# Optimization experiments

Measured on AMD Instinct MI355X. Metric: run time of the kernel, lower is better.

The kernel has to match this reference:

```python
import jax, jax.numpy as jnp
import numpy as np

NUM_GRAPHS = 512

def gcn_conv(x, src, dst, W, b, n):
    # x: [N, Fin], W: [Fin, Fout]. PyG GCNConv: add self loops, symmetric norm.
    h = x @ W  # [N, Fout]
    loop = jnp.arange(n)
    s = jnp.concatenate([src, loop])
    d = jnp.concatenate([dst, loop])
    ones = jnp.ones(s.shape[0], dtype=h.dtype)
    deg = jax.ops.segment_sum(ones, d, num_segments=n)  # includes self loop -> >= 1
    dinv = jax.lax.rsqrt(deg)
    norm = dinv[s] * dinv[d]  # [E+N]
    msg = h[s] * norm[:, None]  # gather + scale (memory-bound)
    out = jax.ops.segment_sum(msg, d, num_segments=n)
    return out + b

def setup_inputs() -> dict:
    key = jax.random.key(0)
    ks = jax.random.split(key, 10)
    N, E, F, H, O, EF = 100000, 1600000, 128, 128, 1, 16
    x = jax.random.normal(ks[0], (N, F), dtype=jnp.float32)
    edge_index = jax.random.randint(ks[1], (2, E), 0, N)
    edge_attr = jax.random.normal(ks[2], (E, EF), dtype=jnp.float32)
    batch = jnp.sort(jax.random.randint(ks[3], (N,), 0, NUM_GRAPHS))
    s1 = 1.0 / np.sqrt(F)
    s2 = 1.0 / np.sqrt(H)
    W1 = jax.random.uniform(ks[4], (F, H), jnp.float32, -s1, s1)
    b1 = jnp.zeros((H,), jnp.float32)
    W2 = jax.random.uniform(ks[5], (H, H), jnp.float32, -s2, s2)
    b2 = jnp.zeros((H,), jnp.float32)
    Wl = jax.random.uniform(ks[6], (H, O), jnp.float32, -s2, s2)
    bl = jnp.zeros((O,), jnp.float32)
    return {"x": x, "edge_index": edge_index, "edge_attr": edge_attr, "batch": batch,
            "W1": W1, "b1": b1, "W2": W2, "b2": b2, "Wl": Wl, "bl": bl}

def reference(x, edge_index, edge_attr, batch, W1, b1, W2, b2, Wl, bl):
    n = x.shape[0]
    src, dst = edge_index[0], edge_index[1]
    h = jax.nn.relu(gcn_conv(x, src, dst, W1, b1, n))
    h = gcn_conv(h, src, dst, W2, b2, n)
    # global mean pool by graph id
    summed = jax.ops.segment_sum(h, batch, num_segments=NUM_GRAPHS)  # [G, H]
    counts = jax.ops.segment_sum(jnp.ones((n,), h.dtype), batch, num_segments=NUM_GRAPHS)
    pooled = summed / jnp.maximum(counts, 1.0)[:, None]
    return pooled @ Wl + bl  # [G, 1]
```

## Files before the change

kernel.cpp:

```cpp
#include <hip/hip_runtime.h>


typedef __attribute__((ext_vector_type(8))) short short8;
typedef __attribute__((ext_vector_type(4))) float f32x4;

#define CHUNK 4096
#define RW    128
#define SCAP  6144
#define JCAP  512
#define WCAP  6144

__device__ __forceinline__ unsigned short bf16r(float f) {
    unsigned u = __float_as_uint(f);
    u += 0x7FFFu + ((u >> 16) & 1u);
    return (unsigned short)(u >> 16);
}

__device__ __forceinline__ float bff(unsigned short u) {
    return __uint_as_float((unsigned)u << 16);
}

__global__ __launch_bounds__(256) void k_partw(
    const int* __restrict__ src, const int* __restrict__ dst,
    int* __restrict__ part, int* __restrict__ off_t, int* __restrict__ cnt_t,
    const float* __restrict__ W1, unsigned short* __restrict__ w1p,
    const float* __restrict__ W2, const float* __restrict__ Wl,
    float* __restrict__ w2l, int E, int nchunks, int NR)
{
    int tid = threadIdx.x;
    if (blockIdx.x >= nchunks) {
        int b = blockIdx.x - nchunks;
        if (b == 64) {
            if (tid < 128) {
                float s = 0.0f;
                for (int j = 0; j < 128; ++j) s = fmaf(W2[tid * 128 + j], Wl[j], s);
                w2l[tid] = s;
            }
            return;
        }
        int idx = b * 256 + tid;
        int k = idx >> 7, n = idx & 127;
        w1p[((k >> 3) * 128 + n) * 8 + (k & 7)] = bf16r(W1[idx]);
        return;
    }

    __shared__ int stage[CHUNK];
    __shared__ int lcnt[1024];
    __shared__ int lscan[1024];
    int j = blockIdx.x;
    int base = j * CHUNK;

#pragma unroll
    for (int k = 0; k < 4; ++k) lcnt[tid + k * 256] = 0;
    __syncthreads();

    int mye[16], myr[16];
#pragma unroll
    for (int k = 0; k < 16; ++k) {
        int e = base + tid + (k << 8);
        bool ok = e < E;
        int s = ok ? src[e] : 0;
        int d = ok ? dst[e] : 0;
        int r = -1;
        if (ok) {
            r = d >> 7;
            atomicAdd(&lcnt[r], 1);
        }
        mye[k] = (s << 7) | (d & 127);
        myr[k] = r;
    }
    __syncthreads();

    int* pa = lcnt;
    int* pb = lscan;
    for (int off = 1; off < 1024; off <<= 1) {
#pragma unroll
        for (int k = 0; k < 4; ++k) {
            int idx = tid + k * 256;
            int v = pa[idx];
            if (idx >= off) v += pa[idx - off];
            pb[idx] = v;
        }
        __syncthreads();
        int* tmp = pa; pa = pb; pb = tmp;
    }
    for (int i = tid; i < NR; i += 256) {
        int incl = pa[i];
        int excl = (i == 0) ? 0 : pa[i - 1];
        pb[i] = excl;
        off_t[(size_t)i * nchunks + j] = excl;
        cnt_t[(size_t)i * nchunks + j] = incl - excl;
    }
    __syncthreads();

#pragma unroll
    for (int k = 0; k < 16; ++k) {
        if (myr[k] >= 0) {
            int p = atomicAdd(&pb[myr[k]], 1);
            stage[p] = mye[k];
        }
    }
    __syncthreads();

    int valid = E - base; if (valid > CHUNK) valid = CHUNK;
    for (int i = tid; i < valid; i += 256)
        part[(size_t)base + i] = stage[i];
}

__global__ __launch_bounds__(256) void k_build(
    const int* __restrict__ part, const int* __restrict__ off_t,
    const int* __restrict__ cnt_t, const float* __restrict__ x,
    const unsigned short* __restrict__ w1p, int* __restrict__ srt,
    int* __restrict__ rps, int* __restrict__ rpe, float* __restrict__ dinv,
    unsigned short* __restrict__ t, int nchunks, int N, int NR)
{
    __shared__ int stage[SCAP];
    __shared__ int jbase[JCAP];
    __shared__ int hist[RW], lcur[RW], s1[RW], s2[RW];
    __shared__ float dins[RW];
    __shared__ int cursor;
    __shared__ unsigned short w1s[16384];
    int r = blockIdx.x;
    int tid = threadIdx.x;
    int d0 = r << 7;
    int width = N - d0; if (width > RW) width = RW;

    {
        const uint4* s = (const uint4*)w1p;
        uint4* d = (uint4*)w1s;
#pragma unroll
        for (int i = 0; i < 8; ++i) d[tid + i * 256] = s[tid + i * 256];
    }
    if (tid < RW) hist[tid] = 0;
    if (tid == 0) cursor = 0;
    __syncthreads();

    const int* orow = off_t + (size_t)r * nchunks;
    const int* crow = cnt_t + (size_t)r * nchunks;

    for (int j = tid; j < nchunks; j += 256) {
        int c = crow[j];
        if (c == 0) { if (j < JCAP) jbase[j] = 0; continue; }
        int b = (j < JCAP) ? atomicAdd(&cursor, c) : SCAP;
        if (j < JCAP) jbase[j] = b;
        const int* pp = part + (size_t)j * CHUNK + orow[j];
        for (int e = 0; e < c; ++e) {
            int ed = pp[e];
            int pos = b + e;
            if (pos < SCAP) stage[pos] = ed;
            atomicAdd(&hist[ed & 127], 1);
        }
    }
    __syncthreads();
    int total = cursor;

    if (tid < RW) s1[tid] = hist[tid];
    __syncthreads();
    int* pa = s1; int* pb = s2;
    for (int off = 1; off < RW; off <<= 1) {
        if (tid < RW) {
            int v = pa[tid];
            if (tid >= off) v += pa[tid - off];
            pb[tid] = v;
        }
        __syncthreads();
        int* tmp = pa; pa = pb; pb = tmp;
    }
    int wbase = r * WCAP;
    if (tid < width) {
        int excl = (tid == 0) ? 0 : pa[tid - 1];
        int start = wbase + excl;
        int deg = hist[tid];
        rps[d0 + tid] = start;
        rpe[d0 + tid] = start + deg;
        lcur[tid] = start;
        float di = 1.0f / sqrtf((float)deg + 1.0f);
        dins[tid] = di;
        dinv[d0 + tid] = di;
    }
    __syncthreads();

    int lim = total < SCAP ? total : SCAP;
    for (int i = tid; i < lim; i += 256) {
        int ed = stage[i];
        int pos = atomicAdd(&lcur[ed & 127], 1);
        srt[pos] = ed >> 7;
    }
    if (total > SCAP || nchunks > JCAP) {
        for (int j = tid; j < nchunks; j += 256) {
            int c = crow[j];
            if (c == 0) continue;
            int e0 = 0;
            if (j < JCAP) {
                int b = jbase[j];
                e0 = SCAP - b;
                if (e0 < 0) e0 = 0;
                if (e0 >= c) continue;
            }
            const int* pp = part + (size_t)j * CHUNK + orow[j];
            for (int e = e0; e < c; ++e) {
                int ed = pp[e];
                int pos = atomicAdd(&lcur[ed & 127], 1);
                srt[pos] = ed >> 7;
            }
        }
    }

    int w = tid >> 6, lane = tid & 63;
    int m = lane & 15, quad = lane >> 4;
    int r0 = d0 + w * 32;

    f32x4 acc[2][8];
#pragma unroll
    for (int rg = 0; rg < 2; ++rg)
#pragma unroll
        for (int cg = 0; cg < 8; ++cg) {
            f32x4 z = {0.0f, 0.0f, 0.0f, 0.0f};
            acc[rg][cg] = z;
        }

#pragma unroll
    for (int ks = 0; ks < 4; ++ks) {
        int k0 = ks * 32 + quad * 8;
        short8 a[2];
#pragma unroll
        for (int rg = 0; rg < 2; ++rg) {
            int rr = r0 + rg * 16 + m;
            if (rr > N - 1) rr = N - 1;
            const float* ap = x + (size_t)rr * 128 + k0;
            float4 v0 = *(const float4*)ap;
            float4 v1 = *(const float4*)(ap + 4);
            short8 av;
            av[0] = (short)bf16r(v0.x); av[1] = (short)bf16r(v0.y);
            av[2] = (short)bf16r(v0.z); av[3] = (short)bf16r(v0.w);
            av[4] = (short)bf16r(v1.x); av[5] = (short)bf16r(v1.y);
            av[6] = (short)bf16r(v1.z); av[7] = (short)bf16r(v1.w);
            a[rg] = av;
        }
        int kc = ks * 4 + quad;
#pragma unroll
        for (int cg = 0; cg < 8; ++cg) {
            const short8* bp = (const short8*)&w1s[((size_t)kc * 128 + cg * 16 + m) * 8];
            short8 b = *bp;
            acc[0][cg] = __builtin_amdgcn_mfma_f32_16x16x32_bf16(a[0], b, acc[0][cg], 0, 0, 0);
            acc[1][cg] = __builtin_amdgcn_mfma_f32_16x16x32_bf16(a[1], b, acc[1][cg], 0, 0, 0);
        }
    }

#pragma unroll
    for (int rg = 0; rg < 2; ++rg) {
        int rb = r0 + rg * 16 + quad * 4;
#pragma unroll
        for (int reg = 0; reg < 4; ++reg) {
            int row = rb + reg;
            if (row < N) {
                float s = dins[row - d0];
#pragma unroll
                for (int cg = 0; cg < 8; ++cg)
                    t[(size_t)row * 128 + cg * 16 + m] = bf16r(acc[rg][cg][reg] * s);
            }
        }
    }

    if (r == NR - 1 && tid < 16) {
        uint4 z = {0u, 0u, 0u, 0u};
        ((uint4*)(t + (size_t)N * 128))[tid] = z;
    }
}

__global__ __launch_bounds__(256) void k_agg1(
    const unsigned short* __restrict__ t, const float* __restrict__ dinv,
    const int* __restrict__ rps, const int* __restrict__ rpe,
    const int* __restrict__ srt,
    const float* __restrict__ b1, const float* __restrict__ w2l,
    float* __restrict__ q, int N, int nwaves)
{
    __shared__ int shi[4][2][64];
    int wave = threadIdx.x >> 6;
    int lane = threadIdx.x & 63;
    int gw = blockIdx.x * 4 + wave;
    if (gw >= N) return;

    int r4 = lane >> 4;
    int c = lane & 15;
    const unsigned short* tc = t + c * 8;

    float4 b0 = *(const float4*)(b1 + c * 8);
    float4 b4 = *(const float4*)(b1 + c * 8 + 4);
    float4 w0 = *(const float4*)(w2l + c * 8);
    float4 w4 = *(const float4*)(w2l + c * 8 + 4);

    int node = gw;
    int s0 = rps[node], s1 = rpe[node];
    float di = dinv[node];
    {
        int deg = s1 - s0;
        int vdeg = deg < 63 ? deg : 63;
        int idx = N;
        if (lane < vdeg) idx = srt[s0 + lane];
        else if (lane == vdeg) idx = node;
        shi[wave][0][lane] = idx;
    }
    int buf = 0;

    while (true) {
        int nnode = node + nwaves;
        int ns0 = 0, ns1 = 0, nidx = N;
        float ndi = 0.0f;
        bool have_next = nnode < N;
        if (have_next) {
            ns0 = rps[nnode]; ns1 = rpe[nnode];
            ndi = dinv[nnode];
            int ndeg = ns1 - ns0;
            int nvdeg = ndeg < 63 ? ndeg : 63;
            if (lane < nvdeg) nidx = srt[ns0 + lane];
            else if (lane == nvdeg) nidx = nnode;
        }

        const int* shw = shi[wave][buf];
        int deg = s1 - s0;
        int vdeg = deg < 63 ? deg : 63;
        float a[8];
#pragma unroll
        for (int k = 0; k < 8; ++k) a[k] = 0.0f;
        int nrows = vdeg + 1;
        int nquads = (nrows + 3) >> 2;
        int p = 0;
        do {
            short8 v[8];
#pragma unroll
            for (int j = 0; j < 8; ++j) {
                int id = shw[((p + j) << 2) + r4];
                v[j] = *(const short8*)(tc + (size_t)id * 128);
            }
#pragma unroll
            for (int j = 0; j < 8; ++j)
#pragma unroll
                for (int k = 0; k < 8; ++k)
                    a[k] += bff((unsigned short)v[j][k]);
            p += 8;
        } while (p < nquads);

        if (deg > 63) {
            for (int e = s0 + 63; e < s1; ++e) {
                int id = srt[e];
                short8 v = *(const short8*)(tc + (size_t)id * 128);
                if (r4 == 0)
#pragma unroll
                    for (int k = 0; k < 8; ++k)
                        a[k] += bff((unsigned short)v[k]);
            }
        }

#pragma unroll
        for (int k = 0; k < 8; ++k) {
            a[k] += __shfl_xor(a[k], 16);
            a[k] += __shfl_xor(a[k], 32);
        }

        float pr = 0.0f;
        pr += fmaxf(fmaf(a[0], di, b0.x), 0.0f) * w0.x;
        pr += fmaxf(fmaf(a[1], di, b0.y), 0.0f) * w0.y;
        pr += fmaxf(fmaf(a[2], di, b0.z), 0.0f) * w0.z;
        pr += fmaxf(fmaf(a[3], di, b0.w), 0.0f) * w0.w;
        pr += fmaxf(fmaf(a[4], di, b4.x), 0.0f) * w4.x;
        pr += fmaxf(fmaf(a[5], di, b4.y), 0.0f) * w4.y;
        pr += fmaxf(fmaf(a[6], di, b4.z), 0.0f) * w4.z;
        pr += fmaxf(fmaf(a[7], di, b4.w), 0.0f) * w4.w;
#pragma unroll
        for (int off = 8; off > 0; off >>= 1) pr += __shfl_xor(pr, off);
        if (lane == 0) q[node] = pr * di;

        if (!have_next) break;
        shi[wave][buf ^ 1][lane] = nidx;
        node = nnode; s0 = ns0; s1 = ns1; di = ndi; buf ^= 1;
    }
}

__global__ __launch_bounds__(256) void k_agg2(
    const float* __restrict__ q, const float* __restrict__ dinv,
    const int* __restrict__ rps, const int* __restrict__ rpe,
    const int* __restrict__ srt, float* __restrict__ p, int N)
{
    int tid = blockIdx.x * 256 + threadIdx.x;
    int node = tid >> 4;
    int l = tid & 15;
    if (node >= N) return;
    int s0 = rps[node], s1 = rpe[node];
    float a = 0.0f;
    for (int e = s0 + l; e < s1; e += 16) a += q[srt[e]];
#pragma unroll
    for (int off = 8; off > 0; off >>= 1) a += __shfl_xor(a, off);
    if (l == 0) p[node] = dinv[node] * (a + q[node]);
}

__global__ __launch_bounds__(64) void k_pool(
    const float* __restrict__ p, const int* __restrict__ batch,
    const float* __restrict__ b2, const float* __restrict__ Wl,
    const float* __restrict__ bl, float* __restrict__ out, int N, int G)
{
    int g = blockIdx.x;
    int lane = threadIdx.x;
    __shared__ int sb[2];
    if (lane < 2) {
        int target = g + lane;
        int lo = 0, hi = N;
        while (lo < hi) {
            int mid = (lo + hi) >> 1;
            if (batch[mid] < target) lo = mid + 1; else hi = mid;
        }
        sb[lane] = lo;
    }
    __syncthreads();
    int s = sb[0], e = sb[1];
    float a = 0.0f;
    for (int i = s + lane; i < e; i += 64) a += p[i];
#pragma unroll
    for (int off = 32; off > 0; off >>= 1) a += __shfl_xor(a, off);
    if (lane == 0) {
        float c = 0.0f;
        for (int j = 0; j < 128; ++j) c = fmaf(b2[j], Wl[j], c);
        out[g] = a / fmaxf((float)(e - s), 1.0f) + c + bl[0];
    }
}

extern "C" void kernel_launch(void* const* d_in, const int* in_sizes, int n_in,
                              void* d_out, int out_size, void* d_ws, size_t ws_size,
                              hipStream_t stream)
{
    const float* x  = (const float*)d_in[0];
    const int*   ei = (const int*)d_in[1];
    const int*   batch = (const int*)d_in[3];
    const float* W1 = (const float*)d_in[4];
    const float* b1 = (const float*)d_in[5];
    const float* W2 = (const float*)d_in[6];
    const float* b2 = (const float*)d_in[7];
    const float* Wl = (const float*)d_in[8];
    const float* bl = (const float*)d_in[9];

    int N = in_sizes[0] / 128;
    int E = in_sizes[1] / 2;
    const int* src = ei;
    const int* dst = ei + E;

    char* ws = (char*)d_ws;
    size_t off = 0;
    auto alloc = [&](size_t bytes) -> void* {
        void* p = ws + off;
        off = (off + bytes + 255) & ~(size_t)255;
        return p;
    };
    int nchunks = (E + CHUNK - 1) / CHUNK;
    int NR = (N + RW - 1) / RW;
    unsigned short* t = (unsigned short*)alloc((size_t)(N + 1) * 128 * 2);
    float* q    = (float*)alloc((size_t)N * 4);
    float* p    = (float*)alloc((size_t)N * 4);
    int*   srt  = (int*)alloc((size_t)NR * WCAP * 4);
    int*   part = (int*)alloc((size_t)nchunks * CHUNK * 4);
    int*   off_t= (int*)alloc((size_t)NR * nchunks * 4);
    int*   cnt_t= (int*)alloc((size_t)NR * nchunks * 4);
    float* dinv = (float*)alloc((size_t)N * 4);
    int*   rps  = (int*)alloc((size_t)N * 4);
    int*   rpe  = (int*)alloc((size_t)N * 4);
    float* w2l  = (float*)alloc(128 * 4);
    unsigned short* w1p = (unsigned short*)alloc(16384 * 2);
    (void)ws_size;

    k_partw<<<nchunks + 65, 256, 0, stream>>>(src, dst, part, off_t, cnt_t,
                                              W1, w1p, W2, Wl, w2l, E, nchunks, NR);
    k_build<<<NR, 256, 0, stream>>>(part, off_t, cnt_t, x, w1p, srt, rps, rpe,
                                    dinv, t, nchunks, N, NR);
    int a1b = 2048;
    k_agg1<<<a1b, 256, 0, stream>>>(t, dinv, rps, rpe, srt, b1, w2l, q, N, a1b * 4);
    k_agg2<<<((size_t)N * 16 + 255) / 256, 256, 0, stream>>>(q, dinv, rps, rpe, srt, p, N);
    k_pool<<<512, 64, 0, stream>>>(p, batch, b2, Wl, bl, (float*)d_out, N, 512);
}
```

Baseline: 332.6 us.

## Slice feature table into 8 column slabs and aggregate per slab

The transformed feature table is stored as 8 slabs of 16 columns each, so each layer-1 aggregation block handles one slab. Each block walks nodes with 8 lanes per neighbor row, which keeps a slab in cache and improves L2 locality of the random gathers. A new reduction kernel sums the 8 partial projection results per node. The build kernel's chunk scan now uses wave-parallel lanes instead of one thread per chunk, and the stage capacity shrinks. The cost is more kernel launches and extra q8 memory traffic, plus index loads repeated once per slab.

```diff
diff --git a/kernel.cpp b/kernel.cpp
--- a/kernel.cpp
+++ b/kernel.cpp
@@ -6,7 +6,7 @@
 
 #define CHUNK 4096
 #define RW    128
-#define SCAP  6144
+#define SCAP  4096
 #define JCAP  512
 #define WCAP  6144
 
@@ -112,7 +112,7 @@
     const int* __restrict__ cnt_t, const float* __restrict__ x,
     const unsigned short* __restrict__ w1p, int* __restrict__ srt,
     int* __restrict__ rps, int* __restrict__ rpe, float* __restrict__ dinv,
-    unsigned short* __restrict__ t, int nchunks, int N, int NR)
+    unsigned short* __restrict__ t8, int nchunks, int N, int NR)
 {
     __shared__ int stage[SCAP];
     __shared__ int jbase[JCAP];
@@ -122,6 +122,7 @@
     __shared__ unsigned short w1s[16384];
     int r = blockIdx.x;
     int tid = threadIdx.x;
+    int wave = tid >> 6, lane = tid & 63;
     int d0 = r << 7;
     int width = N - d0; if (width > RW) width = RW;
 
@@ -138,13 +139,17 @@
     const int* orow = off_t + (size_t)r * nchunks;
     const int* crow = cnt_t + (size_t)r * nchunks;
 
-    for (int j = tid; j < nchunks; j += 256) {
+    for (int j = wave; j < nchunks; j += 4) {
         int c = crow[j];
-        if (c == 0) { if (j < JCAP) jbase[j] = 0; continue; }
-        int b = (j < JCAP) ? atomicAdd(&cursor, c) : SCAP;
-        if (j < JCAP) jbase[j] = b;
+        if (c == 0) { if (lane == 0 && j < JCAP) jbase[j] = 0; continue; }
+        int b = 0;
+        if (lane == 0) {
+            b = atomicAdd(&cursor, c);
+            if (j < JCAP) jbase[j] = b;
+        }
+        b = __shfl(b, 0);
         const int* pp = part + (size_t)j * CHUNK + orow[j];
-        for (int e = 0; e < c; ++e) {
+        for (int e = lane; e < c; e += 64) {
             int ed = pp[e];
             int pos = b + e;
             if (pos < SCAP) stage[pos] = ed;
@@ -206,7 +211,7 @@
         }
     }
 
-    int w = tid >> 6, lane = tid & 63;
+    int w = wave;
     int m = lane & 15, quad = lane >> 4;
     int r0 = d0 + w * 32;
 
@@ -257,123 +262,82 @@
                 float s = dins[row - d0];
 #pragma unroll
                 for (int cg = 0; cg < 8; ++cg)
-                    t[(size_t)row * 128 + cg * 16 + m] = bf16r(acc[rg][cg][reg] * s);
+                    t8[((size_t)cg * (N + 1) + row) * 16 + m] =
+                        bf16r(acc[rg][cg][reg] * s);
             }
         }
     }
 
     if (r == NR - 1 && tid < 16) {
+        int sl = tid >> 1, half = tid & 1;
         uint4 z = {0u, 0u, 0u, 0u};
-        ((uint4*)(t + (size_t)N * 128))[tid] = z;
+        *(uint4*)(t8 + ((size_t)sl * (N + 1) + N) * 16 + half * 8) = z;
     }
 }
 
 __global__ __launch_bounds__(256) void k_agg1(
-    const unsigned short* __restrict__ t, const float* __restrict__ dinv,
+    const unsigned short* __restrict__ t8, const float* __restrict__ dinv,
     const int* __restrict__ rps, const int* __restrict__ rpe,
-    const int* __restrict__ srt,
-    const float* __restrict__ b1, const float* __restrict__ w2l,
-    float* __restrict__ q, int N, int nwaves)
-{
-    __shared__ int shi[4][2][64];
-    int wave = threadIdx.x >> 6;
-    int lane = threadIdx.x & 63;
-    int gw = blockIdx.x * 4 + wave;
-    if (gw >= N) return;
-
-    int r4 = lane >> 4;
-    int c = lane & 15;
-    const unsigned short* tc = t + c * 8;
-
-    float4 b0 = *(const float4*)(b1 + c * 8);
-    float4 b4 = *(const float4*)(b1 + c * 8 + 4);
-    float4 w0 = *(const float4*)(w2l + c * 8);
-    float4 w4 = *(const float4*)(w2l + c * 8 + 4);
-
-    int node = gw;
-    int s0 = rps[node], s1 = rpe[node];
-    float di = dinv[node];
-    {
+    const int* __restrict__ srt, const float* __restrict__ b1,
+    const float* __restrict__ w2l, float* __restrict__ q8, int N, int gstride)
+{
+    int wave = threadIdx.x >> 6, lane = threadIdx.x & 63;
+    int sl = blockIdx.x & 7;
+    int wg = (blockIdx.x >> 3) * 4 + wave;
+    int f2 = lane & 7;
+    const unsigned short* tbase = t8 + (size_t)sl * (N + 1) * 16 + f2 * 2;
+    float2 bb = *(const float2*)(b1 + sl * 16 + f2 * 2);
+    float2 ww = *(const float2*)(w2l + sl * 16 + f2 * 2);
+    float* qout = q8 + (size_t)sl * N;
+
+    for (int node = wg; node < N; node += gstride) {
+        int s0 = rps[node], s1 = rpe[node];
         int deg = s1 - s0;
         int vdeg = deg < 63 ? deg : 63;
         int idx = N;
         if (lane < vdeg) idx = srt[s0 + lane];
         else if (lane == vdeg) idx = node;
-        shi[wave][0][lane] = idx;
-    }
-    int buf = 0;
-
-    while (true) {
-        int nnode = node + nwaves;
-        int ns0 = 0, ns1 = 0, nidx = N;
-        float ndi = 0.0f;
-        bool have_next = nnode < N;
-        if (have_next) {
-            ns0 = rps[nnode]; ns1 = rpe[nnode];
-            ndi = dinv[nnode];
-            int ndeg = ns1 - ns0;
-            int nvdeg = ndeg < 63 ? ndeg : 63;
-            if (lane < nvdeg) nidx = srt[ns0 + lane];
-            else if (lane == nvdeg) nidx = nnode;
-        }
-
-        const int* shw = shi[wave][buf];
-        int deg = s1 - s0;
-        int vdeg = deg < 63 ? deg : 63;
-        float a[8];
-#pragma unroll
-        for (int k = 0; k < 8; ++k) a[k] = 0.0f;
-        int nrows = vdeg + 1;
-        int nquads = (nrows + 3) >> 2;
-        int p = 0;
-        do {
-            short8 v[8];
-#pragma unroll
-            for (int j = 0; j < 8; ++j) {
-                int id = shw[((p + j) << 2) + r4];
-                v[j] = *(const short8*)(tc + (size_t)id * 128);
-            }
-#pragma unroll
-            for (int j = 0; j < 8; ++j)
-#pragma unroll
-                for (int k = 0; k < 8; ++k)
-                    a[k] += bff((unsigned short)v[j][k]);
-            p += 8;
-        } while (p < nquads);
-
+        float a0 = 0.0f, a1 = 0.0f;
+        int nb = (vdeg + 8) >> 3;
+        for (int b = 0; b < nb; ++b) {
+            int id = __shfl(idx, (b << 3) + (lane >> 3));
+            unsigned u = *(const unsigned*)(tbase + (size_t)id * 16);
+            a0 += bff((unsigned short)(u & 0xffff));
+            a1 += bff((unsigned short)(u >> 16));
+        }
         if (deg > 63) {
             for (int e = s0 + 63; e < s1; ++e) {
                 int id = srt[e];
-                short8 v = *(const short8*)(tc + (size_t)id * 128);
-                if (r4 == 0)
-#pragma unroll
-                    for (int k = 0; k < 8; ++k)
-                        a[k] += bff((unsigned short)v[k]);
+                if (lane < 8) {
+                    unsigned u = *(const unsigned*)(tbase + (size_t)id * 16);
+                    a0 += bff((unsigned short)(u & 0xffff));
+                    a1 += bff((unsigned short)(u >> 16));
+                }
             }
         }
-
-#pragma unroll
-        for (int k = 0; k < 8; ++k) {
-            a[k] += __shfl_xor(a[k], 16);
-            a[k] += __shfl_xor(a[k], 32);
-        }
-
-        float pr = 0.0f;
-        pr += fmaxf(fmaf(a[0], di, b0.x), 0.0f) * w0.x;
-        pr += fmaxf(fmaf(a[1], di, b0.y), 0.0f) * w0.y;
-        pr += fmaxf(fmaf(a[2], di, b0.z), 0.0f) * w0.z;
-        pr += fmaxf(fmaf(a[3], di, b0.w), 0.0f) * w0.w;
-        pr += fmaxf(fmaf(a[4], di, b4.x), 0.0f) * w4.x;
-        pr += fmaxf(fmaf(a[5], di, b4.y), 0.0f) * w4.y;
-        pr += fmaxf(fmaf(a[6], di, b4.z), 0.0f) * w4.z;
-        pr += fmaxf(fmaf(a[7], di, b4.w), 0.0f) * w4.w;
-#pragma unroll
-        for (int off = 8; off > 0; off >>= 1) pr += __shfl_xor(pr, off);
-        if (lane == 0) q[node] = pr * di;
-
-        if (!have_next) break;
-        shi[wave][buf ^ 1][lane] = nidx;
-        node = nnode; s0 = ns0; s1 = ns1; di = ndi; buf ^= 1;
+        a0 += __shfl_xor(a0, 8);  a1 += __shfl_xor(a1, 8);
+        a0 += __shfl_xor(a0, 16); a1 += __shfl_xor(a1, 16);
+        a0 += __shfl_xor(a0, 32); a1 += __shfl_xor(a1, 32);
+        float di = dinv[node];
+        float h0 = fmaxf(fmaf(a0, di, bb.x), 0.0f);
+        float h1 = fmaxf(fmaf(a1, di, bb.y), 0.0f);
+        float pr = h0 * ww.x + h1 * ww.y;
+        pr += __shfl_xor(pr, 1);
+        pr += __shfl_xor(pr, 2);
+        pr += __shfl_xor(pr, 4);
+        if (lane == 0) qout[node] = pr * di;
+    }
+}
+
+__global__ __launch_bounds__(256) void k_qred(
+    const float* __restrict__ q8, float* __restrict__ q, int N)
+{
+    int i = blockIdx.x * 256 + threadIdx.x;
+    if (i < N) {
+        float s = 0.0f;
+#pragma unroll
+        for (int sl = 0; sl < 8; ++sl) s += q8[(size_t)sl * N + i];
+        q[i] = s;
     }
 }
 
@@ -452,7 +416,8 @@
     };
     int nchunks = (E + CHUNK - 1) / CHUNK;
     int NR = (N + RW - 1) / RW;
-    unsigned short* t = (unsigned short*)alloc((size_t)(N + 1) * 128 * 2);
+    unsigned short* t8 = (unsigned short*)alloc((size_t)8 * (N + 1) * 16 * 2);
+    float* q8   = (float*)alloc((size_t)8 * N * 4);
     float* q    = (float*)alloc((size_t)N * 4);
     float* p    = (float*)alloc((size_t)N * 4);
     int*   srt  = (int*)alloc((size_t)NR * WCAP * 4);
@@ -469,9 +434,11 @@
     k_partw<<<nchunks + 65, 256, 0, stream>>>(src, dst, part, off_t, cnt_t,
                                               W1, w1p, W2, Wl, w2l, E, nchunks, NR);
     k_build<<<NR, 256, 0, stream>>>(part, off_t, cnt_t, x, w1p, srt, rps, rpe,
-                                    dinv, t, nchunks, N, NR);
+                                    dinv, t8, nchunks, N, NR);
     int a1b = 2048;
-    k_agg1<<<a1b, 256, 0, stream>>>(t, dinv, rps, rpe, srt, b1, w2l, q, N, a1b * 4);
+    k_agg1<<<a1b, 256, 0, stream>>>(t8, dinv, rps, rpe, srt, b1, w2l, q8, N,
+                                    (a1b / 8) * 4);
+    k_qred<<<(N + 255) / 256, 256, 0, stream>>>(q8, q, N);
     k_agg2<<<((size_t)N * 16 + 255) / 256, 256, 0, stream>>>(q, dinv, rps, rpe, srt, p, N);
     k_pool<<<512, 64, 0, stream>>>(p, batch, b2, Wl, bl, (float*)d_out, N, 512);
 }
```

New measurement: 571.8 us. 1.72x slower.

## Shrink partition chunks, alias build LDS, and use one-node-per-wave agg1

Applied to the files above, without the earlier changes.

Halves the edge-partition chunk size so k_partw launches more blocks with fewer registers per thread, and raises JCAP so every chunk fits in the shared jbase table. k_build now reuses one shared buffer for the staging area and the bf16 W1 tile, loading W1 only after the sort finishes; this cuts its LDS footprint so more blocks can sit on a CU. k_agg1 drops its persistent grid-stride loop with index prefetch double-buffering and launches one wave per node, with 8/4/2/1 tail unrolling so low-degree nodes no longer load eight padded quads. In exchange it loses the prefetch overlap, adds barriers to k_build, and doubles the number of off_t/cnt_t entries.

```diff
diff --git a/kernel.cpp b/kernel.cpp
--- a/kernel.cpp
+++ b/kernel.cpp
@@ -4,10 +4,10 @@
 typedef __attribute__((ext_vector_type(8))) short short8;
 typedef __attribute__((ext_vector_type(4))) float f32x4;
 
-#define CHUNK 4096
+#define CHUNK 2048
 #define RW    128
 #define SCAP  6144
-#define JCAP  512
+#define JCAP  1024
 #define WCAP  6144
 
 __device__ __forceinline__ unsigned short bf16r(float f) {
@@ -54,9 +54,9 @@
     for (int k = 0; k < 4; ++k) lcnt[tid + k * 256] = 0;
     __syncthreads();
 
-    int mye[16], myr[16];
-#pragma unroll
-    for (int k = 0; k < 16; ++k) {
+    int mye[8], myr[8];
+#pragma unroll
+    for (int k = 0; k < 8; ++k) {
         int e = base + tid + (k << 8);
         bool ok = e < E;
         int s = ok ? src[e] : 0;
@@ -94,7 +94,7 @@
     __syncthreads();
 
 #pragma unroll
-    for (int k = 0; k < 16; ++k) {
+    for (int k = 0; k < 8; ++k) {
         if (myr[k] >= 0) {
             int p = atomicAdd(&pb[myr[k]], 1);
             stage[p] = mye[k];
@@ -114,23 +114,17 @@
     int* __restrict__ rps, int* __restrict__ rpe, float* __restrict__ dinv,
     unsigned short* __restrict__ t, int nchunks, int N, int NR)
 {
-    __shared__ int stage[SCAP];
-    __shared__ int jbase[JCAP];
+    __shared__ int shu[8192];
     __shared__ int hist[RW], lcur[RW], s1[RW], s2[RW];
     __shared__ float dins[RW];
     __shared__ int cursor;
-    __shared__ unsigned short w1s[16384];
+    int* stage = shu;
+    int* jbase = shu + SCAP;
     int r = blockIdx.x;
     int tid = threadIdx.x;
     int d0 = r << 7;
     int width = N - d0; if (width > RW) width = RW;
 
-    {
-        const uint4* s = (const uint4*)w1p;
-        uint4* d = (uint4*)w1s;
-#pragma unroll
-        for (int i = 0; i < 8; ++i) d[tid + i * 256] = s[tid + i * 256];
-    }
     if (tid < RW) hist[tid] = 0;
     if (tid == 0) cursor = 0;
     __syncthreads();
@@ -140,9 +134,9 @@
 
     for (int j = tid; j < nchunks; j += 256) {
         int c = crow[j];
-        if (c == 0) { if (j < JCAP) jbase[j] = 0; continue; }
-        int b = (j < JCAP) ? atomicAdd(&cursor, c) : SCAP;
-        if (j < JCAP) jbase[j] = b;
+        if (c == 0) { jbase[j] = 0; continue; }
+        int b = atomicAdd(&cursor, c);
+        jbase[j] = b;
         const int* pp = part + (size_t)j * CHUNK + orow[j];
         for (int e = 0; e < c; ++e) {
             int ed = pp[e];
@@ -186,17 +180,14 @@
         int pos = atomicAdd(&lcur[ed & 127], 1);
         srt[pos] = ed >> 7;
     }
-    if (total > SCAP || nchunks > JCAP) {
+    if (total > SCAP) {
         for (int j = tid; j < nchunks; j += 256) {
             int c = crow[j];
             if (c == 0) continue;
-            int e0 = 0;
-            if (j < JCAP) {
-                int b = jbase[j];
-                e0 = SCAP - b;
-                if (e0 < 0) e0 = 0;
-                if (e0 >= c) continue;
-            }
+            int b = jbase[j];
+            int e0 = SCAP - b;
+            if (e0 < 0) e0 = 0;
+            if (e0 >= c) continue;
             const int* pp = part + (size_t)j * CHUNK + orow[j];
             for (int e = e0; e < c; ++e) {
                 int ed = pp[e];
@@ -205,6 +196,16 @@
             }
         }
     }
+    __syncthreads();
+
+    unsigned short* w1s = (unsigned short*)shu;
+    {
+        const uint4* s = (const uint4*)w1p;
+        uint4* d = (uint4*)shu;
+#pragma unroll
+        for (int i = 0; i < 8; ++i) d[tid + i * 256] = s[tid + i * 256];
+    }
+    __syncthreads();
 
     int w = tid >> 6, lane = tid & 63;
     int m = lane & 15, quad = lane >> 4;
@@ -273,108 +274,118 @@
     const int* __restrict__ rps, const int* __restrict__ rpe,
     const int* __restrict__ srt,
     const float* __restrict__ b1, const float* __restrict__ w2l,
-    float* __restrict__ q, int N, int nwaves)
-{
-    __shared__ int shi[4][2][64];
+    float* __restrict__ q, int N)
+{
+    __shared__ int shi[4][64];
     int wave = threadIdx.x >> 6;
     int lane = threadIdx.x & 63;
-    int gw = blockIdx.x * 4 + wave;
-    if (gw >= N) return;
+    int node = blockIdx.x * 4 + wave;
+    if (node >= N) return;
+    int s0 = rps[node], s1 = rpe[node];
+    int deg = s1 - s0;
+    int vdeg = deg < 63 ? deg : 63;
+
+    int idx = N;
+    if (lane < vdeg) idx = srt[s0 + lane];
+    else if (lane == vdeg) idx = node;
+    shi[wave][lane] = idx;
+    const int* shw = shi[wave];
 
     int r4 = lane >> 4;
     int c = lane & 15;
     const unsigned short* tc = t + c * 8;
 
+    float a[8];
+#pragma unroll
+    for (int k = 0; k < 8; ++k) a[k] = 0.0f;
+
+    int nrows = vdeg + 1;
+    int nquads = (nrows + 3) >> 2;
+    int p = 0;
+
+    while (p + 8 <= nquads) {
+        short8 v[8];
+#pragma unroll
+        for (int j = 0; j < 8; ++j) {
+            int id = shw[((p + j) << 2) + r4];
+            v[j] = *(const short8*)(tc + (size_t)id * 128);
+        }
+#pragma unroll
+        for (int j = 0; j < 8; ++j)
+#pragma unroll
+            for (int k = 0; k < 8; ++k)
+                a[k] += bff((unsigned short)v[j][k]);
+        p += 8;
+    }
+    if (p + 4 <= nquads) {
+        short8 v[4];
+#pragma unroll
+        for (int j = 0; j < 4; ++j) {
+            int id = shw[((p + j) << 2) + r4];
+            v[j] = *(const short8*)(tc + (size_t)id * 128);
+        }
+#pragma unroll
+        for (int j = 0; j < 4; ++j)
+#pragma unroll
+            for (int k = 0; k < 8; ++k)
+                a[k] += bff((unsigned short)v[j][k]);
+        p += 4;
+    }
+    if (p + 2 <= nquads) {
+        short8 v[2];
+#pragma unroll
+        for (int j = 0; j < 2; ++j) {
+            int id = shw[((p + j) << 2) + r4];
+            v[j] = *(const short8*)(tc + (size_t)id * 128);
+        }
+#pragma unroll
+        for (int j = 0; j < 2; ++j)
+#pragma unroll
+            for (int k = 0; k < 8; ++k)
+                a[k] += bff((unsigned short)v[j][k]);
+        p += 2;
+    }
+    if (p < nquads) {
+        int id = shw[(p << 2) + r4];
+        short8 v = *(const short8*)(tc + (size_t)id * 128);
+#pragma unroll
+        for (int k = 0; k < 8; ++k)
+            a[k] += bff((unsigned short)v[k]);
+    }
+    if (deg > 63) {
+        for (int e = s0 + 63; e < s1; ++e) {
+            int id = srt[e];
+            short8 v = *(const short8*)(tc + (size_t)id * 128);
+            if (r4 == 0)
+#pragma unroll
+                for (int k = 0; k < 8; ++k)
+                    a[k] += bff((unsigned short)v[k]);
+        }
+    }
+
+#pragma unroll
+    for (int k = 0; k < 8; ++k) {
+        a[k] += __shfl_xor(a[k], 16);
+        a[k] += __shfl_xor(a[k], 32);
+    }
+
+    float di = dinv[node];
     float4 b0 = *(const float4*)(b1 + c * 8);
     float4 b4 = *(const float4*)(b1 + c * 8 + 4);
     float4 w0 = *(const float4*)(w2l + c * 8);
     float4 w4 = *(const float4*)(w2l + c * 8 + 4);
-
-    int node = gw;
-    int s0 = rps[node], s1 = rpe[node];
-    float di = dinv[node];
-    {
-        int deg = s1 - s0;
-        int vdeg = deg < 63 ? deg : 63;
-        int idx = N;
-        if (lane < vdeg) idx = srt[s0 + lane];
-        else if (lane == vdeg) idx = node;
-        shi[wave][0][lane] = idx;
-    }
-    int buf = 0;
-
-    while (true) {
-        int nnode = node + nwaves;
-        int ns0 = 0, ns1 = 0, nidx = N;
-        float ndi = 0.0f;
-        bool have_next = nnode < N;
-        if (have_next) {
-            ns0 = rps[nnode]; ns1 = rpe[nnode];
-            ndi = dinv[nnode];
-            int ndeg = ns1 - ns0;
-            int nvdeg = ndeg < 63 ? ndeg : 63;
-            if (lane < nvdeg) nidx = srt[ns0 + lane];
-            else if (lane == nvdeg) nidx = nnode;
-        }
-
-        const int* shw = shi[wave][buf];
-        int deg = s1 - s0;
-        int vdeg = deg < 63 ? deg : 63;
-        float a[8];
-#pragma unroll
-        for (int k = 0; k < 8; ++k) a[k] = 0.0f;
-        int nrows = vdeg + 1;
-        int nquads = (nrows + 3) >> 2;
-        int p = 0;
-        do {
-            short8 v[8];
-#pragma unroll
-            for (int j = 0; j < 8; ++j) {
-                int id = shw[((p + j) << 2) + r4];
-                v[j] = *(const short8*)(tc + (size_t)id * 128);
-            }
-#pragma unroll
-            for (int j = 0; j < 8; ++j)
-#pragma unroll
-                for (int k = 0; k < 8; ++k)
-                    a[k] += bff((unsigned short)v[j][k]);
-            p += 8;
-        } while (p < nquads);
-
-        if (deg > 63) {
-            for (int e = s0 + 63; e < s1; ++e) {
-                int id = srt[e];
-                short8 v = *(const short8*)(tc + (size_t)id * 128);
-                if (r4 == 0)
-#pragma unroll
-                    for (int k = 0; k < 8; ++k)
-                        a[k] += bff((unsigned short)v[k]);
-            }
-        }
-
-#pragma unroll
-        for (int k = 0; k < 8; ++k) {
-            a[k] += __shfl_xor(a[k], 16);
-            a[k] += __shfl_xor(a[k], 32);
-        }
-
-        float pr = 0.0f;
-        pr += fmaxf(fmaf(a[0], di, b0.x), 0.0f) * w0.x;
-        pr += fmaxf(fmaf(a[1], di, b0.y), 0.0f) * w0.y;
-        pr += fmaxf(fmaf(a[2], di, b0.z), 0.0f) * w0.z;
-        pr += fmaxf(fmaf(a[3], di, b0.w), 0.0f) * w0.w;
-        pr += fmaxf(fmaf(a[4], di, b4.x), 0.0f) * w4.x;
-        pr += fmaxf(fmaf(a[5], di, b4.y), 0.0f) * w4.y;
-        pr += fmaxf(fmaf(a[6], di, b4.z), 0.0f) * w4.z;
-        pr += fmaxf(fmaf(a[7], di, b4.w), 0.0f) * w4.w;
-#pragma unroll
-        for (int off = 8; off > 0; off >>= 1) pr += __shfl_xor(pr, off);
-        if (lane == 0) q[node] = pr * di;
-
-        if (!have_next) break;
-        shi[wave][buf ^ 1][lane] = nidx;
-        node = nnode; s0 = ns0; s1 = ns1; di = ndi; buf ^= 1;
-    }
+    float pr = 0.0f;
+    pr += fmaxf(fmaf(a[0], di, b0.x), 0.0f) * w0.x;
+    pr += fmaxf(fmaf(a[1], di, b0.y), 0.0f) * w0.y;
+    pr += fmaxf(fmaf(a[2], di, b0.z), 0.0f) * w0.z;
+    pr += fmaxf(fmaf(a[3], di, b0.w), 0.0f) * w0.w;
+    pr += fmaxf(fmaf(a[4], di, b4.x), 0.0f) * w4.x;
+    pr += fmaxf(fmaf(a[5], di, b4.y), 0.0f) * w4.y;
+    pr += fmaxf(fmaf(a[6], di, b4.z), 0.0f) * w4.z;
+    pr += fmaxf(fmaf(a[7], di, b4.w), 0.0f) * w4.w;
+#pragma unroll
+    for (int off = 8; off > 0; off >>= 1) pr += __shfl_xor(pr, off);
+    if (lane == 0) q[node] = pr * di;
 }
 
 __global__ __launch_bounds__(256) void k_agg2(
@@ -470,8 +481,7 @@
                                               W1, w1p, W2, Wl, w2l, E, nchunks, NR);
     k_build<<<NR, 256, 0, stream>>>(part, off_t, cnt_t, x, w1p, srt, rps, rpe,
                                     dinv, t, nchunks, N, NR);
-    int a1b = 2048;
-    k_agg1<<<a1b, 256, 0, stream>>>(t, dinv, rps, rpe, srt, b1, w2l, q, N, a1b * 4);
+    k_agg1<<<(N + 3) / 4, 256, 0, stream>>>(t, dinv, rps, rpe, srt, b1, w2l, q, N);
     k_agg2<<<((size_t)N * 16 + 255) / 256, 256, 0, stream>>>(q, dinv, rps, rpe, srt, p, N);
     k_pool<<<512, 64, 0, stream>>>(p, batch, b2, Wl, bl, (float*)d_out, N, 512);
 }
```

New measurement: 324.9 us. 1.02x faster.
